# Performance work log

Hardware: AMD Instinct MI355X
Metric: run time of the kernel (lower is better)

The kernel has to match this reference:

```python
import jax, jax.numpy as jnp
import numpy as np

B, L, C = 256, 256, 128
HID, H = 128, 4
D = HID // H            # 32
NUM_LAYERS = 2
NEG_SLOPE = 0.2
LN_EPS = 1e-5


def setup_inputs() -> dict:
    key = jax.random.key(0)
    ks = jax.random.split(key, 16)
    E = 4096
    x = jax.random.normal(ks[0], (B, L, C), dtype=jnp.float32)
    edge_index = jax.random.randint(ks[1], (2, E), 0, C, dtype=jnp.int64)
    s_in = 1.0 / np.sqrt(L)
    s_h = 1.0 / np.sqrt(HID)
    return {
        "x": x,
        "edge_index": edge_index,
        "emb_W": jax.random.normal(ks[2], (L, HID), jnp.float32) * s_in,
        "emb_b": jnp.zeros((HID,), jnp.float32),
        "lin_l_W": jax.random.normal(ks[3], (NUM_LAYERS, HID, HID), jnp.float32) * s_h,
        "lin_l_b": jnp.zeros((NUM_LAYERS, HID), jnp.float32),
        "lin_r_W": jax.random.normal(ks[4], (NUM_LAYERS, HID, HID), jnp.float32) * s_h,
        "lin_r_b": jnp.zeros((NUM_LAYERS, HID), jnp.float32),
        "att": jax.random.normal(ks[5], (NUM_LAYERS, H, D), jnp.float32) * (1.0 / np.sqrt(D)),
        "gat_bias": jnp.zeros((NUM_LAYERS, HID), jnp.float32),
        "ln_gamma": jnp.ones((NUM_LAYERS, HID), jnp.float32),
        "ln_beta": jnp.zeros((NUM_LAYERS, HID), jnp.float32),
        "proj_W": jax.random.normal(ks[6], (HID, L), jnp.float32) * s_h,
        "proj_b": jnp.zeros((L,), jnp.float32),
    }


def _batch_edges(edge_index):
    # replicate single-graph edges per batch sample with node offsets, then add self loops
    E = edge_index.shape[1]
    off = jnp.repeat(jnp.arange(B, dtype=edge_index.dtype) * C, E)
    src = jnp.tile(edge_index[0], B) + off
    dst = jnp.tile(edge_index[1], B) + off
    loop = jnp.arange(B * C, dtype=edge_index.dtype)
    return jnp.concatenate([src, loop]), jnp.concatenate([dst, loop])


def _layer_norm(x, g, b):
    mu = jnp.mean(x, axis=-1, keepdims=True)
    var = jnp.mean(jnp.square(x - mu), axis=-1, keepdims=True)
    return (x - mu) * jax.lax.rsqrt(var + LN_EPS) * g + b


def _gatv2(x, src, dst, Wl, bl, Wr, br, a, bias):
    N = x.shape[0]
    xl = (x @ Wl + bl).reshape(N, H, D)   # source-side transform
    xr = (x @ Wr + br).reshape(N, H, D)   # target-side transform
    e = jax.nn.leaky_relu(xl[src] + xr[dst], NEG_SLOPE)   # (E', H, D)
    logits = jnp.einsum('ehd,hd->eh', e, a)               # (E', H)
    m = jax.ops.segment_max(logits, dst, num_segments=N)
    p = jnp.exp(logits - m[dst])
    s = jax.ops.segment_sum(p, dst, num_segments=N)
    alpha = p / (s[dst] + 1e-16)
    out = jax.ops.segment_sum(xl[src] * alpha[:, :, None], dst, num_segments=N)
    return out.reshape(N, HID) + bias, alpha


def reference(x, edge_index, emb_W, emb_b, lin_l_W, lin_l_b, lin_r_W, lin_r_b,
              att, gat_bias, ln_gamma, ln_beta, proj_W, proj_b):
    src, dst = _batch_edges(edge_index)
    # (B, L, C) -> nodes are channels: (B*C, L) -> embed to HID
    h = x.transpose(0, 2, 1).reshape(B * C, L) @ emb_W + emb_b
    alpha = None
    for i in range(NUM_LAYERS):
        new_h, alpha = _gatv2(h, src, dst, lin_l_W[i], lin_l_b[i],
                              lin_r_W[i], lin_r_b[i], att[i], gat_bias[i])
        new_h = jax.nn.elu(new_h)
        h = h + new_h
        h = _layer_norm(h, ln_gamma[i], ln_beta[i])
        # dropout: eval mode, identity
    # attention map (to_dense_adj semantics: adj[b, src%C, dst%C] = mean_h(alpha), then transpose)
    b_idx = src // C
    dense = jnp.zeros((B, C, C), x.dtype).at[b_idx, src % C, dst % C].add(alpha.mean(axis=-1))
    attn_map = dense.transpose(0, 2, 1)
    out = (h @ proj_W + proj_b).reshape(B, C, L).transpose(0, 2, 1)  # (B, L, C)
    return out, attn_map
```

## Files before the change

### kernel.cpp

```cpp
#include <hip/hip_runtime.h>
#include <hip/hip_fp16.h>
#include <math.h>

#define BB 256
#define LL 256
#define CC 128
#define HIDD 128
#define HH 4
#define DD 32
#define EE 4096
#define NN (BB*CC)
#define LN_EPS 1e-5f

typedef short bf16x8 __attribute__((ext_vector_type(8)));
typedef _Float16 f16x8 __attribute__((ext_vector_type(8)));
typedef float f32x4 __attribute__((ext_vector_type(4)));

__device__ __forceinline__ float red64(float p) {
    p += __shfl_xor(p, 32);
    p += __shfl_xor(p, 16);
    p += __shfl_xor(p, 8);
    p += __shfl_xor(p, 4);
    p += __shfl_xor(p, 2);
    p += __shfl_xor(p, 1);
    return p;
}
__device__ __forceinline__ unsigned bfr(float f) {
    unsigned x = __float_as_uint(f);
    return (x + 0x7FFFu + ((x >> 16) & 1u)) >> 16;
}
__device__ __forceinline__ unsigned pack2(float a, float b) { return bfr(a) | (bfr(b) << 16); }
__device__ __forceinline__ float b2f(unsigned u) { return __uint_as_float(u << 16); }

__device__ __forceinline__ void stage_bf16_rm(ushort* lds, const ushort* src, int ldm, int t) {
    #pragma unroll
    for (int i = 0; i < 8; ++i) {
        int flat = i*256 + t;
        int r = flat >> 4, c = flat & 15;
        uint4 pk = *(const uint4*)(src + (size_t)r*ldm + c*8);
        *(uint4*)&lds[((r*16) + (c ^ (r & 7)))*8] = pk;
    }
}
__device__ __forceinline__ void mfma_tile_128(const ushort* Als, const ushort* Bls,
                                              f32x4 acc[2][8], int w, int lane) {
    int mr = lane & 15, quad = lane >> 4;
    #pragma unroll
    for (int ks = 0; ks < 4; ++ks) {
        int ca = ks*4 + quad;
        bf16x8 a[2], b[8];
        #pragma unroll
        for (int mf = 0; mf < 2; ++mf) {
            int m = w*32 + mf*16 + mr;
            a[mf] = *(const bf16x8*)&Als[((m*16) + (ca ^ (m & 7)))*8];
        }
        #pragma unroll
        for (int nf = 0; nf < 8; ++nf) {
            int n = nf*16 + mr;
            b[nf] = *(const bf16x8*)&Bls[((n*16) + (ca ^ (n & 7)))*8];
        }
        #pragma unroll
        for (int mf = 0; mf < 2; ++mf)
            #pragma unroll
            for (int nf = 0; nf < 8; ++nf)
                acc[mf][nf] = __builtin_amdgcn_mfma_f32_16x16x32_bf16(a[mf], b[nf], acc[mf][nf], 0, 0, 0);
    }
}
#define ZERO_ACC(acc) { _Pragma("unroll") for (int i_=0;i_<2;++i_) { _Pragma("unroll") for (int j_=0;j_<8;++j_) acc[i_][j_] = (f32x4){0.f,0.f,0.f,0.f}; } }

__global__ __launch_bounds__(256) void prep_weights(const float* __restrict__ emb_W,
                                                    const float* __restrict__ lWl,
                                                    const float* __restrict__ lWr,
                                                    const float* __restrict__ pW,
                                                    const int* __restrict__ edge,
                                                    ushort* __restrict__ WembT,
                                                    ushort* __restrict__ WlrT,
                                                    ushort* __restrict__ WpT,
                                                    __half* __restrict__ mult_ds) {
    __shared__ int cnt[CC*CC];
    int t = threadIdx.x;
    if (blockIdx.x == 64) {
        for (int i = t; i < CC*CC; i += 256) cnt[i] = 0;
        __syncthreads();
        for (int j = t; j < EE; j += 256) {
            int s = edge[j], d = edge[EE + j];
            atomicAdd(&cnt[s*CC + d], 1);
        }
        __syncthreads();
        for (int o = t; o < CC*CC; o += 256) {
            int dstc = o >> 7, srcc = o & 127;
            int c = cnt[srcc*CC + dstc] + ((srcc == dstc) ? 1 : 0);
            mult_ds[o] = __float2half((float)c);
        }
        return;
    }
    int gid = blockIdx.x * 256 + t;
    float v[8];
    if (gid < 4096) {
        int f = gid >> 5, ch = gid & 31;
        #pragma unroll
        for (int j = 0; j < 8; ++j) v[j] = emb_W[(size_t)(ch*8 + j)*HIDD + f];
        uint4 pk; pk.x = pack2(v[0],v[1]); pk.y = pack2(v[2],v[3]);
        pk.z = pack2(v[4],v[5]); pk.w = pack2(v[6],v[7]);
        *(uint4*)&WembT[(size_t)f*LL + ch*8] = pk;
    } else if (gid < 12288) {
        int g = gid - 4096;
        int mat = g >> 11, f = (g >> 4) & 127, ch = g & 15;
        const float* src = ((mat & 1) ? lWr : lWl) + (size_t)(mat >> 1)*HIDD*HIDD;
        #pragma unroll
        for (int j = 0; j < 8; ++j) v[j] = src[(size_t)(ch*8 + j)*HIDD + f];
        uint4 pk; pk.x = pack2(v[0],v[1]); pk.y = pack2(v[2],v[3]);
        pk.z = pack2(v[4],v[5]); pk.w = pack2(v[6],v[7]);
        *(uint4*)&WlrT[(size_t)mat*HIDD*HIDD + (size_t)f*HIDD + ch*8] = pk;
    } else {
        int g = gid - 12288;
        int l = g >> 4, ch = g & 15;
        #pragma unroll
        for (int j = 0; j < 8; ++j) v[j] = pW[(size_t)(ch*8 + j)*LL + l];
        uint4 pk; pk.x = pack2(v[0],v[1]); pk.y = pack2(v[2],v[3]);
        pk.z = pack2(v[4],v[5]); pk.w = pack2(v[6],v[7]);
        *(uint4*)&WpT[(size_t)l*HIDD + ch*8] = pk;
    }
}

__global__ __launch_bounds__(256) void embed_mfma(const float* __restrict__ x,
                                                  const ushort* __restrict__ WembT,
                                                  const float* __restrict__ bias,
                                                  ushort* __restrict__ hout) {
    __shared__ __align__(16) ushort Als[128*16*8];
    __shared__ __align__(16) ushort Bls[128*16*8];
    int b = blockIdx.x;
    int t = threadIdx.x, lane = t & 63, w = t >> 6;
    f32x4 acc[2][8];
    ZERO_ACC(acc)
    #pragma unroll
    for (int kh = 0; kh < 2; ++kh) {
        if (kh) __syncthreads();
        const float4* x4 = (const float4*)(x + (size_t)b*LL*CC + (size_t)kh*128*CC);
        int rot = (t >> 3) & 3;
        #pragma unroll
        for (int i = 0; i < 8; ++i) {
            int flat = i*256 + t;
            int lp = flat >> 5, c4 = flat & 31;
            float4 v0 = x4[(size_t)(2*lp)*32 + c4];
            float4 v1 = x4[(size_t)(2*lp + 1)*32 + c4];
            int lc = lp >> 2, lh = lp & 3;
            #pragma unroll
            for (int j0 = 0; j0 < 4; ++j0) {
                int j = (j0 + rot) & 3;
                int c = c4*4 + j;
                unsigned pk = pack2(((const float*)&v0)[j], ((const float*)&v1)[j]);
                *(unsigned*)&Als[((c*16) + (lc ^ (c & 7)))*8 + lh*2] = pk;
            }
        }
        stage_bf16_rm(Bls, WembT + kh*128, LL, t);
        __syncthreads();
        mfma_tile_128(Als, Bls, acc, w, lane);
    }
    int mr = lane & 15, quad = lane >> 4;
    #pragma unroll
    for (int nf = 0; nf < 8; ++nf) {
        int f = nf*16 + mr;
        float bv = bias[f];
        #pragma unroll
        for (int mf = 0; mf < 2; ++mf)
            #pragma unroll
            for (int r = 0; r < 4; ++r) {
                int node = w*32 + mf*16 + quad*4 + r;
                hout[((size_t)b*CC + node)*HIDD + f] = (ushort)bfr(acc[mf][nf][r] + bv);
            }
    }
}

__global__ __launch_bounds__(256) void lin_mfma(const ushort* __restrict__ hmat,
                                                const ushort* __restrict__ WlT,
                                                const ushort* __restrict__ WrT,
                                                const float* __restrict__ bl,
                                                const float* __restrict__ br,
                                                __half* __restrict__ xlT,
                                                __half* __restrict__ xrT) {
    __shared__ __align__(16) ushort Als[128*16*8];
    __shared__ __align__(16) ushort Bls[128*16*8];
    int b = blockIdx.x;
    int t = threadIdx.x, lane = t & 63, w = t >> 6;
    int mr = lane & 15, quad = lane >> 4;
    stage_bf16_rm(Als, hmat + (size_t)b*CC*HIDD, HIDD, t);
    #pragma unroll
    for (int lr = 0; lr < 2; ++lr) {
        if (lr) __syncthreads();
        stage_bf16_rm(Bls, lr ? WrT : WlT, HIDD, t);
        __syncthreads();
        f32x4 acc[2][8];
        ZERO_ACC(acc)
        mfma_tile_128(Als, Bls, acc, w, lane);
        const float* bias = lr ? br : bl;
        __half* out = lr ? xrT : xlT;
        #pragma unroll
        for (int nf = 0; nf < 8; ++nf) {
            int f = nf*16 + mr;
            float bv = bias[f];
            int h = f >> 5, d = f & 31;
            #pragma unroll
            for (int mf = 0; mf < 2; ++mf)
                #pragma unroll
                for (int r = 0; r < 4; ++r) {
                    int node = w*32 + mf*16 + quad*4 + r;
                    out[(((size_t)b*HH + h)*CC + node)*DD + d] = __float2half(acc[mf][nf][r] + bv);
                }
        }
    }
}

#define SLOT(q, mr) ((mr)*4 + (((q) ^ (mr) ^ ((mr) >> 2)) & 3))

__global__ __launch_bounds__(256) __attribute__((amdgpu_waves_per_eu(4, 4)))
void gat_fused(const __half* __restrict__ xl_h,
               const __half* __restrict__ xr_h,
               const __half* __restrict__ mult_ds,
               const float* __restrict__ att,
               __half* __restrict__ xagg,
               __half* __restrict__ Pg) {
    __shared__ __align__(16) __half smemA[CC*CC];
    __shared__ __align__(16) __half xlT_swz[DD*16*8];
    __half* xl_lds = smemA;
    float*  Slq    = (float*)(smemA + CC*DD);
    float*  rp     = Slq + CC;
    float*  sp     = rp + 4*CC;
    __half* Pfrag  = smemA;

    int bh = blockIdx.x;
    int h = bh & 3, b = bh >> 2;
    int t = threadIdx.x;
    int sg = t >> 6, dl = t & 63;
    int dstA = dl, dstB = dl + 64;

    {
        const uint4* spg = (const uint4*)(xl_h + (size_t)bh * CC * DD);
        uint4* dp = (uint4*)xl_lds;
        dp[t] = spg[t];
        dp[t + 256] = spg[t + 256];
    }
    __half2 qa2[16];
    const float* ag = att + h*DD;
    #pragma unroll
    for (int c = 0; c < 8; ++c) {
        float4 av = *(const float4*)&ag[c*4];
        qa2[2*c+0] = __floats2half2_rn(0.4f*av.x, 0.4f*av.y);
        qa2[2*c+1] = __floats2half2_rn(0.4f*av.z, 0.4f*av.w);
    }
    __half2 xrA[16], xrB[16];
    float fSA, fSB;
    {
        uint4 XA[4], XB[4];
        const uint4* pa = (const uint4*)(xr_h + ((size_t)bh*CC + dstA)*DD);
        const uint4* pb = (const uint4*)(xr_h + ((size_t)bh*CC + dstB)*DD);
        #pragma unroll
        for (int c = 0; c < 4; ++c) { XA[c] = pa[c]; XB[c] = pb[c]; }
        const __half2* va = (const __half2*)XA;
        const __half2* vb = (const __half2*)XB;
        float sA = 0.f, sB = 0.f;
        #pragma unroll
        for (int i = 0; i < 16; ++i) {
            xrA[i] = va[i]; xrB[i] = vb[i];
            __half2 p = __hmul2(qa2[i], xrA[i]);
            sA += __low2float(p) + __high2float(p);
            __half2 q = __hmul2(qa2[i], xrB[i]);
            sB += __low2float(q) + __high2float(q);
        }
        fSA = 1.5f * sA; fSB = 1.5f * sB;
    }
    __syncthreads();

    if (t < CC) {
        uint4 R[4];
        const uint4* rpt = (const uint4*)&xl_lds[t*DD];
        #pragma unroll
        for (int c = 0; c < 4; ++c) R[c] = rpt[c];
        const __half2* rv = (const __half2*)R;
        __half2 s = __floats2half2_rn(0.f, 0.f);
        #pragma unroll
        for (int i = 0; i < 16; ++i) s = __hfma2(qa2[i], rv[i], s);
        Slq[t] = 1.5f * (__low2float(s) + __high2float(s));
    }
    for (int i = t; i < 512; i += 256) {
        int f = i & 31, c = i >> 5;
        __align__(16) __half v[8];
        #pragma unroll
        for (int e = 0; e < 8; ++e) v[e] = xl_lds[(c*8 + e)*DD + f];
        *(uint4*)&xlT_swz[((f*16) + (c ^ (f & 7)))*8] = *(uint4*)v;
    }
    __syncthreads();

    __half2 lvA[16], lvB[16];
    float pmA0 = -3.0e38f, pmA1 = pmA0, pmB0 = pmA0, pmB1 = pmA0;
    float lbufA = 0.f, lbufB = 0.f;
    #pragma unroll
    for (int j = 0; j < 32; ++j) {
        int src = sg*32 + j;
        uint4 R[4];
        const uint4* rpt = (const uint4*)&xl_lds[src*DD];
        R[0] = rpt[0]; R[1] = rpt[1]; R[2] = rpt[2]; R[3] = rpt[3];
        float sl = Slq[src];
        const __half2* xv = (const __half2*)R;
        __half2 a0 = __floats2half2_rn(0.f,0.f), a1 = a0, a2 = a0, a3 = a0;
        __half2 b0 = a0, b1 = a0, b2 = a0, b3 = a0;
        #pragma unroll
        for (int q = 0; q < 4; ++q) {
            a0 = __hfma2(qa2[4*q+0], __habs2(__hadd2(xv[4*q+0], xrA[4*q+0])), a0);
            a1 = __hfma2(qa2[4*q+1], __habs2(__hadd2(xv[4*q+1], xrA[4*q+1])), a1);
            a2 = __hfma2(qa2[4*q+2], __habs2(__hadd2(xv[4*q+2], xrA[4*q+2])), a2);
            a3 = __hfma2(qa2[4*q+3], __habs2(__hadd2(xv[4*q+3], xrA[4*q+3])), a3);
            b0 = __hfma2(qa2[4*q+0], __habs2(__hadd2(xv[4*q+0], xrB[4*q+0])), b0);
            b1 = __hfma2(qa2[4*q+1], __habs2(__hadd2(xv[4*q+1], xrB[4*q+1])), b1);
            b2 = __hfma2(qa2[4*q+2], __habs2(__hadd2(xv[4*q+2], xrB[4*q+2])), b2);
            b3 = __hfma2(qa2[4*q+3], __habs2(__hadd2(xv[4*q+3], xrB[4*q+3])), b3);
        }
        __half2 tsA = __hadd2(__hadd2(a0, a1), __hadd2(a2, a3));
        __half2 tsB = __hadd2(__hadd2(b0, b1), __hadd2(b2, b3));
        float lA = (fSA + sl) + (__low2float(tsA) + __high2float(tsA));
        float lB = (fSB + sl) + (__low2float(tsB) + __high2float(tsB));
        if (j & 1) {
            pmA1 = fmaxf(pmA1, lA); pmB1 = fmaxf(pmB1, lB);
            lvA[j >> 1] = __floats2half2_rn(lbufA, lA);
            lvB[j >> 1] = __floats2half2_rn(lbufB, lB);
        } else {
            pmA0 = fmaxf(pmA0, lA); pmB0 = fmaxf(pmB0, lB);
            lbufA = lA; lbufB = lB;
        }
    }
    rp[sg*CC + dstA] = fmaxf(pmA0, pmA1);
    rp[sg*CC + dstB] = fmaxf(pmB0, pmB1);
    __syncthreads();
    float mA = fmaxf(fmaxf(rp[0*CC + dstA], rp[1*CC + dstA]),
                     fmaxf(rp[2*CC + dstA], rp[3*CC + dstA]));
    float mB = fmaxf(fmaxf(rp[0*CC + dstB], rp[1*CC + dstB]),
                     fmaxf(rp[2*CC + dstB], rp[3*CC + dstB]));

    uint4 MAr[4], MBr[4];
    {
        const uint4* ma = (const uint4*)(mult_ds + (size_t)dstA*CC + sg*32);
        const uint4* mb = (const uint4*)(mult_ds + (size_t)dstB*CC + sg*32);
        #pragma unroll
        for (int c = 0; c < 4; ++c) { MAr[c] = ma[c]; MBr[c] = mb[c]; }
    }
    const __half* multA = (const __half*)MAr;
    const __half* multB = (const __half*)MBr;

    float sA0 = 0.f, sA1 = 0.f, sB0 = 0.f, sB1 = 0.f;
    #pragma unroll
    for (int i = 0; i < 16; ++i) {
        float eA0 = __expf(__low2float(lvA[i]) - mA) * __half2float(multA[2*i]);
        float eA1 = __expf(__high2float(lvA[i]) - mA) * __half2float(multA[2*i+1]);
        float eB0 = __expf(__low2float(lvB[i]) - mB) * __half2float(multB[2*i]);
        float eB1 = __expf(__high2float(lvB[i]) - mB) * __half2float(multB[2*i+1]);
        if (i & 1) { sA1 += eA0 + eA1; sB1 += eB0 + eB1; }
        else       { sA0 += eA0 + eA1; sB0 += eB0 + eB1; }
        lvA[i] = __floats2half2_rn(eA0, eA1);
        lvB[i] = __floats2half2_rn(eB0, eB1);
    }
    sp[sg*CC + dstA] = sA0 + sA1;
    sp[sg*CC + dstB] = sB0 + sB1;
    __syncthreads();
    float isA = 1.f / (((sp[0*CC + dstA] + sp[1*CC + dstA]) +
                        (sp[2*CC + dstA] + sp[3*CC + dstA])) + 1e-16f);
    float isB = 1.f / (((sp[0*CC + dstB] + sp[1*CC + dstB]) +
                        (sp[2*CC + dstB] + sp[3*CC + dstB])) + 1e-16f);
    __syncthreads();

    {
        int mr = dl & 15, dr0 = dl >> 4;
        __half* pfA = &Pfrag[(((dr0    )*4 + sg)*64)*8];
        __half* pfB = &Pfrag[(((dr0 + 4)*4 + sg)*64)*8];
        __half* pgA = Pg ? Pg + (size_t)bh*CC*CC + (size_t)dstA*CC + sg*32 : nullptr;
        __half* pgB = Pg ? Pg + (size_t)bh*CC*CC + (size_t)dstB*CC + sg*32 : nullptr;
        #pragma unroll
        for (int q = 0; q < 4; ++q) {
            __align__(16) __half ovA[8], ovB[8];
            #pragma unroll
            for (int i = 0; i < 4; ++i) {
                __half2 vA = lvA[q*4 + i], vB = lvB[q*4 + i];
                ovA[2*i+0] = __float2half(__low2float(vA) * isA);
                ovA[2*i+1] = __float2half(__high2float(vA) * isA);
                ovB[2*i+0] = __float2half(__low2float(vB) * isB);
                ovB[2*i+1] = __float2half(__high2float(vB) * isB);
            }
            *(uint4*)&pfA[SLOT(q, mr)*8] = *(uint4*)ovA;
            *(uint4*)&pfB[SLOT(q, mr)*8] = *(uint4*)ovB;
            if (pgA) {
                *(uint4*)&pgA[q*8] = *(uint4*)ovA;
                *(uint4*)&pgB[q*8] = *(uint4*)ovB;
            }
        }
    }
    __syncthreads();

    int quad = dl >> 4, mr = dl & 15;
    f16x8 afr[2][4];
    #pragma unroll
    for (int mf = 0; mf < 2; ++mf) {
        int dr0 = sg*2 + mf;
        #pragma unroll
        for (int ks = 0; ks < 4; ++ks)
            afr[mf][ks] = *(const f16x8*)&Pfrag[((dr0*4 + ks)*64 + SLOT(quad, mr))*8];
    }
    f32x4 acc[2][2];
    #pragma unroll
    for (int i = 0; i < 2; ++i)
        #pragma unroll
        for (int j = 0; j < 2; ++j) acc[i][j] = (f32x4){0.f,0.f,0.f,0.f};
    #pragma unroll
    for (int ks = 0; ks < 4; ++ks) {
        int ca = ks*4 + quad;
        f16x8 bfr2[2];
        #pragma unroll
        for (int nf = 0; nf < 2; ++nf) {
            int n = nf*16 + mr;
            bfr2[nf] = *(const f16x8*)&xlT_swz[((n*16) + (ca ^ (n & 7)))*8];
        }
        #pragma unroll
        for (int mf = 0; mf < 2; ++mf)
            #pragma unroll
            for (int nf = 0; nf < 2; ++nf)
                acc[mf][nf] = __builtin_amdgcn_mfma_f32_16x16x32_f16(afr[mf][ks], bfr2[nf], acc[mf][nf], 0, 0, 0);
    }
    #pragma unroll
    for (int mf = 0; mf < 2; ++mf)
        #pragma unroll
        for (int nf = 0; nf < 2; ++nf) {
            int f = nf*16 + mr;
            #pragma unroll
            for (int r = 0; r < 4; ++r) {
                int node = sg*32 + mf*16 + quad*4 + r;
                xagg[(((size_t)b*CC + node)*HH + h)*DD + f] = __float2half(acc[mf][nf][r]);
            }
        }
}

__global__ __launch_bounds__(256) void gat_epilogue(const __half* __restrict__ xagg,
                                                    const float* __restrict__ gbias,
                                                    const float* __restrict__ ln_g,
                                                    const float* __restrict__ ln_b,
                                                    const __half* __restrict__ Pws,
                                                    ushort* __restrict__ hmat,
                                                    float* __restrict__ attn_out) {
    int t = threadIdx.x;
    int w = t >> 6, lane = t & 63;
    int node = blockIdx.x*4 + w;
    int b = node >> 7, dstc = node & 127;
    int f0 = lane*2;

    __half2 xa = *(const __half2*)&xagg[(size_t)node*HIDD + f0];
    unsigned hp = *(const unsigned*)&hmat[(size_t)node*HIDD + f0];
    float2 gb = *(const float2*)&gbias[f0];
    float o0 = __low2float(xa) + gb.x;
    float o1 = __high2float(xa) + gb.y;
    o0 = o0 > 0.f ? o0 : (__expf(o0) - 1.f);
    o1 = o1 > 0.f ? o1 : (__expf(o1) - 1.f);
    float hv0 = b2f(hp & 0xFFFFu) + o0;
    float hv1 = b2f(hp >> 16) + o1;

    float mean = red64(hv0 + hv1) * 0.0078125f;
    float d0 = hv0 - mean, d1 = hv1 - mean;
    float var = red64(d0*d0 + d1*d1) * 0.0078125f;
    float rs = rsqrtf(var + LN_EPS);
    float2 g2 = *(const float2*)&ln_g[f0];
    float2 be = *(const float2*)&ln_b[f0];
    *(unsigned*)&hmat[(size_t)node*HIDD + f0] =
        pack2(d0*rs*g2.x + be.x, d1*rs*g2.y + be.y);

    if (attn_out) {
        float a0 = 0.f, a1 = 0.f;
        #pragma unroll
        for (int hh = 0; hh < HH; ++hh) {
            __half2 v = *(const __half2*)&Pws[((size_t)(b*HH + hh)*CC + dstc)*CC + f0];
            a0 += __low2float(v);
            a1 += __high2float(v);
        }
        float2 o; o.x = 0.25f*a0; o.y = 0.25f*a1;
        *(float2*)&attn_out[(size_t)node*CC + f0] = o;
    }
}

__global__ __launch_bounds__(256) void proj_mfma(const ushort* __restrict__ hmat,
                                                 const ushort* __restrict__ WpT,
                                                 const float* __restrict__ bias,
                                                 float* __restrict__ out) {
    __shared__ __align__(16) ushort Als[128*16*8];
    __shared__ __align__(16) ushort Bls[128*16*8];
    int l0 = blockIdx.x * 128;
    int b  = blockIdx.y;
    int t = threadIdx.x, lane = t & 63, w = t >> 6;
    f32x4 acc[2][8];
    ZERO_ACC(acc)
    stage_bf16_rm(Als, WpT + (size_t)l0*HIDD, HIDD, t);
    stage_bf16_rm(Bls, hmat + (size_t)b*CC*HIDD, HIDD, t);
    __syncthreads();
    mfma_tile_128(Als, Bls, acc, w, lane);
    int mr = lane & 15, quad = lane >> 4;
    #pragma unroll
    for (int nf = 0; nf < 8; ++nf) {
        int c = nf*16 + mr;
        #pragma unroll
        for (int mf = 0; mf < 2; ++mf)
            #pragma unroll
            for (int r = 0; r < 4; ++r) {
                int l = l0 + w*32 + mf*16 + quad*4 + r;
                out[((size_t)b*LL + l)*CC + c] = acc[mf][nf][r] + bias[l];
            }
    }
}

extern "C" void kernel_launch(void* const* d_in, const int* in_sizes, int n_in,
                              void* d_out, int out_size, void* d_ws, size_t ws_size,
                              hipStream_t stream) {
    const float* x        = (const float*)d_in[0];
    const int*   edge     = (const int*)d_in[1];
    const float* emb_W    = (const float*)d_in[2];
    const float* emb_b    = (const float*)d_in[3];
    const float* lin_l_W  = (const float*)d_in[4];
    const float* lin_l_b  = (const float*)d_in[5];
    const float* lin_r_W  = (const float*)d_in[6];
    const float* lin_r_b  = (const float*)d_in[7];
    const float* att      = (const float*)d_in[8];
    const float* gat_bias = (const float*)d_in[9];
    const float* ln_g     = (const float*)d_in[10];
    const float* ln_b     = (const float*)d_in[11];
    const float* proj_W   = (const float*)d_in[12];
    const float* proj_b   = (const float*)d_in[13];

    ushort* h     = (ushort*)d_ws;
    __half* xl_h  = (__half*)(h + (size_t)NN * HIDD);
    __half* xr_h  = xl_h + (size_t)NN * HIDD;
    __half* xagg  = xr_h + (size_t)NN * HIDD;
    __half* Pg    = xagg + (size_t)NN * HIDD;
    __half* mult_ds = Pg + (size_t)BB * HH * CC * CC;
    ushort* WembT = (ushort*)(mult_ds + (size_t)CC * CC);
    ushort* WlrT  = WembT + (size_t)CC*LL;
    ushort* WpT   = WlrT + (size_t)4*HIDD*HIDD;

    float* out0 = (float*)d_out;
    float* attn = out0 + (size_t)BB * LL * CC;

    prep_weights<<<65, 256, 0, stream>>>(emb_W, lin_l_W, lin_r_W, proj_W, edge,
                                         WembT, WlrT, WpT, mult_ds);
    embed_mfma<<<BB, 256, 0, stream>>>(x, WembT, emb_b, h);
    for (int layer = 0; layer < 2; ++layer) {
        lin_mfma<<<BB, 256, 0, stream>>>(h,
            WlrT + (size_t)(layer*2 + 0)*HIDD*HIDD,
            WlrT + (size_t)(layer*2 + 1)*HIDD*HIDD,
            lin_l_b + layer*HIDD, lin_r_b + layer*HIDD,
            xl_h, xr_h);
        gat_fused<<<BB*HH, 256, 0, stream>>>(xl_h, xr_h, mult_ds,
            att + layer*HIDD, xagg, (layer == 1) ? Pg : nullptr);
        gat_epilogue<<<NN/4, 256, 0, stream>>>(xagg,
            gat_bias + layer*HIDD, ln_g + layer*HIDD, ln_b + layer*HIDD,
            (layer == 1) ? Pg : nullptr, h, (layer == 1) ? attn : nullptr);
    }
    proj_mfma<<<dim3(2, BB), 256, 0, stream>>>(h, WpT, proj_b, out0);
}
```

Measured before the change: 288.3 us.

## Fuse GAT epilogue LayerNorm into following linear and projection kernels

Result: slower. 401.5 us (+39.3%).

```diff
diff --git a/kernel.cpp b/kernel.cpp
--- a/kernel.cpp
+++ b/kernel.cpp
@@ -16,15 +16,6 @@
 typedef _Float16 f16x8 __attribute__((ext_vector_type(8)));
 typedef float f32x4 __attribute__((ext_vector_type(4)));
 
-__device__ __forceinline__ float red64(float p) {
-    p += __shfl_xor(p, 32);
-    p += __shfl_xor(p, 16);
-    p += __shfl_xor(p, 8);
-    p += __shfl_xor(p, 4);
-    p += __shfl_xor(p, 2);
-    p += __shfl_xor(p, 1);
-    return p;
-}
 __device__ __forceinline__ unsigned bfr(float f) {
     unsigned x = __float_as_uint(f);
     return (x + 0x7FFFu + ((x >> 16) & 1u)) >> 16;
@@ -66,6 +57,75 @@
     }
 }
 #define ZERO_ACC(acc) { _Pragma("unroll") for (int i_=0;i_<2;++i_) { _Pragma("unroll") for (int j_=0;j_<8;++j_) acc[i_][j_] = (f32x4){0.f,0.f,0.f,0.f}; } }
+
+__device__ __forceinline__ void epilogue_to_tile(const __half* __restrict__ xagg,
+                                                 const float* __restrict__ gbias,
+                                                 const float* __restrict__ ln_g,
+                                                 const float* __restrict__ ln_b,
+                                                 ushort* __restrict__ hmat,
+                                                 ushort* __restrict__ tile,
+                                                 int b, int t, bool write_h) {
+    int nl = t >> 1, fh = t & 1;
+    int node = b*CC + nl;
+    const __half* xa = xagg + (size_t)node*HIDD + fh*64;
+    ushort* hp = hmat + (size_t)node*HIDD + fh*64;
+    const float* gb = gbias + fh*64;
+
+    __half2 hv[32];
+    float sum = 0.f;
+    #pragma unroll
+    for (int c = 0; c < 8; ++c) {
+        uint4 xu = *(const uint4*)&xa[c*8];
+        uint4 hu = *(const uint4*)&hp[c*8];
+        const __half2* xp2 = (const __half2*)&xu;
+        const ushort* hs = (const ushort*)&hu;
+        float gv[8];
+        *(float4*)&gv[0] = *(const float4*)&gb[c*8];
+        *(float4*)&gv[4] = *(const float4*)&gb[c*8 + 4];
+        #pragma unroll
+        for (int i = 0; i < 4; ++i) {
+            float o0 = __low2float(xp2[i]) + gv[2*i];
+            float o1 = __high2float(xp2[i]) + gv[2*i+1];
+            o0 = o0 > 0.f ? o0 : (__expf(o0) - 1.f);
+            o1 = o1 > 0.f ? o1 : (__expf(o1) - 1.f);
+            float v0 = b2f((unsigned)hs[2*i]) + o0;
+            float v1 = b2f((unsigned)hs[2*i+1]) + o1;
+            sum += v0 + v1;
+            hv[c*4 + i] = __floats2half2_rn(v0, v1);
+        }
+    }
+    float mean = (sum + __shfl_xor(sum, 1)) * 0.0078125f;
+    float q = 0.f;
+    #pragma unroll
+    for (int i = 0; i < 32; ++i) {
+        float d0 = __low2float(hv[i]) - mean;
+        float d1 = __high2float(hv[i]) - mean;
+        q += d0*d0 + d1*d1;
+    }
+    float var = (q + __shfl_xor(q, 1)) * 0.0078125f;
+    float rs = rsqrtf(var + LN_EPS);
+    const float* lg = ln_g + fh*64;
+    const float* lb = ln_b + fh*64;
+    #pragma unroll
+    for (int c = 0; c < 8; ++c) {
+        float gv[8], bv[8];
+        *(float4*)&gv[0] = *(const float4*)&lg[c*8];
+        *(float4*)&gv[4] = *(const float4*)&lg[c*8 + 4];
+        *(float4*)&bv[0] = *(const float4*)&lb[c*8];
+        *(float4*)&bv[4] = *(const float4*)&lb[c*8 + 4];
+        __align__(16) ushort ov[8];
+        #pragma unroll
+        for (int i = 0; i < 4; ++i) {
+            float d0 = __low2float(hv[c*4 + i]) - mean;
+            float d1 = __high2float(hv[c*4 + i]) - mean;
+            ov[2*i]   = (ushort)bfr(d0*rs*gv[2*i]   + bv[2*i]);
+            ov[2*i+1] = (ushort)bfr(d1*rs*gv[2*i+1] + bv[2*i+1]);
+        }
+        int cg = fh*8 + c;
+        *(uint4*)&tile[((nl*16) + (cg ^ (nl & 7)))*8] = *(uint4*)ov;
+        if (write_h) *(uint4*)&hp[c*8] = *(uint4*)ov;
+    }
+}
 
 __global__ __launch_bounds__(256) void prep_weights(const float* __restrict__ emb_W,
                                                     const float* __restrict__ lWl,
@@ -171,6 +231,38 @@
     }
 }
 
+__device__ __forceinline__ void lin_body(ushort* Als, ushort* Bls,
+                                         const ushort* WlT, const ushort* WrT,
+                                         const float* bl, const float* br,
+                                         __half* xlT, __half* xrT, int b, int t) {
+    int lane = t & 63, w = t >> 6;
+    int mr = lane & 15, quad = lane >> 4;
+    #pragma unroll
+    for (int lr = 0; lr < 2; ++lr) {
+        if (lr) __syncthreads();
+        stage_bf16_rm(Bls, lr ? WrT : WlT, HIDD, t);
+        __syncthreads();
+        f32x4 acc[2][8];
+        ZERO_ACC(acc)
+        mfma_tile_128(Als, Bls, acc, w, lane);
+        const float* bias = lr ? br : bl;
+        __half* out = lr ? xrT : xlT;
+        #pragma unroll
+        for (int nf = 0; nf < 8; ++nf) {
+            int f = nf*16 + mr;
+            float bv = bias[f];
+            int h = f >> 5, d = f & 31;
+            #pragma unroll
+            for (int mf = 0; mf < 2; ++mf)
+                #pragma unroll
+                for (int r = 0; r < 4; ++r) {
+                    int node = w*32 + mf*16 + quad*4 + r;
+                    out[(((size_t)b*HH + h)*CC + node)*DD + d] = __float2half(acc[mf][nf][r] + bv);
+                }
+        }
+    }
+}
+
 __global__ __launch_bounds__(256) void lin_mfma(const ushort* __restrict__ hmat,
                                                 const ushort* __restrict__ WlT,
                                                 const ushort* __restrict__ WrT,
@@ -180,39 +272,32 @@
                                                 __half* __restrict__ xrT) {
     __shared__ __align__(16) ushort Als[128*16*8];
     __shared__ __align__(16) ushort Bls[128*16*8];
-    int b = blockIdx.x;
-    int t = threadIdx.x, lane = t & 63, w = t >> 6;
-    int mr = lane & 15, quad = lane >> 4;
+    int b = blockIdx.x, t = threadIdx.x;
     stage_bf16_rm(Als, hmat + (size_t)b*CC*HIDD, HIDD, t);
-    #pragma unroll
-    for (int lr = 0; lr < 2; ++lr) {
-        if (lr) __syncthreads();
-        stage_bf16_rm(Bls, lr ? WrT : WlT, HIDD, t);
-        __syncthreads();
-        f32x4 acc[2][8];
-        ZERO_ACC(acc)
-        mfma_tile_128(Als, Bls, acc, w, lane);
-        const float* bias = lr ? br : bl;
-        __half* out = lr ? xrT : xlT;
-        #pragma unroll
-        for (int nf = 0; nf < 8; ++nf) {
-            int f = nf*16 + mr;
-            float bv = bias[f];
-            int h = f >> 5, d = f & 31;
-            #pragma unroll
-            for (int mf = 0; mf < 2; ++mf)
-                #pragma unroll
-                for (int r = 0; r < 4; ++r) {
-                    int node = w*32 + mf*16 + quad*4 + r;
-                    out[(((size_t)b*HH + h)*CC + node)*DD + d] = __float2half(acc[mf][nf][r] + bv);
-                }
-        }
-    }
+    lin_body(Als, Bls, WlT, WrT, bl, br, xlT, xrT, b, t);
+}
+
+__global__ __launch_bounds__(256) void epi_lin(const __half* __restrict__ xagg,
+                                               const float* __restrict__ gbias,
+                                               const float* __restrict__ ln_g,
+                                               const float* __restrict__ ln_b,
+                                               const ushort* __restrict__ WlT,
+                                               const ushort* __restrict__ WrT,
+                                               const float* __restrict__ bl,
+                                               const float* __restrict__ br,
+                                               ushort* __restrict__ hmat,
+                                               __half* __restrict__ xlT,
+                                               __half* __restrict__ xrT) {
+    __shared__ __align__(16) ushort Als[128*16*8];
+    __shared__ __align__(16) ushort Bls[128*16*8];
+    int b = blockIdx.x, t = threadIdx.x;
+    epilogue_to_tile(xagg, gbias, ln_g, ln_b, hmat, Als, b, t, true);
+    lin_body(Als, Bls, WlT, WrT, bl, br, xlT, xrT, b, t);
 }
 
 #define SLOT(q, mr) ((mr)*4 + (((q) ^ (mr) ^ ((mr) >> 2)) & 3))
 
-__global__ __launch_bounds__(256) __attribute__((amdgpu_waves_per_eu(4, 4)))
+__global__ __launch_bounds__(256) __attribute__((amdgpu_num_vgpr(128)))
 void gat_fused(const __half* __restrict__ xl_h,
                const __half* __restrict__ xr_h,
                const __half* __restrict__ mult_ds,
@@ -435,77 +520,66 @@
         }
 }
 
-__global__ __launch_bounds__(256) void gat_epilogue(const __half* __restrict__ xagg,
-                                                    const float* __restrict__ gbias,
-                                                    const float* __restrict__ ln_g,
-                                                    const float* __restrict__ ln_b,
-                                                    const __half* __restrict__ Pws,
-                                                    ushort* __restrict__ hmat,
-                                                    float* __restrict__ attn_out) {
-    int t = threadIdx.x;
-    int w = t >> 6, lane = t & 63;
-    int node = blockIdx.x*4 + w;
-    int b = node >> 7, dstc = node & 127;
-    int f0 = lane*2;
-
-    __half2 xa = *(const __half2*)&xagg[(size_t)node*HIDD + f0];
-    unsigned hp = *(const unsigned*)&hmat[(size_t)node*HIDD + f0];
-    float2 gb = *(const float2*)&gbias[f0];
-    float o0 = __low2float(xa) + gb.x;
-    float o1 = __high2float(xa) + gb.y;
-    o0 = o0 > 0.f ? o0 : (__expf(o0) - 1.f);
-    o1 = o1 > 0.f ? o1 : (__expf(o1) - 1.f);
-    float hv0 = b2f(hp & 0xFFFFu) + o0;
-    float hv1 = b2f(hp >> 16) + o1;
-
-    float mean = red64(hv0 + hv1) * 0.0078125f;
-    float d0 = hv0 - mean, d1 = hv1 - mean;
-    float var = red64(d0*d0 + d1*d1) * 0.0078125f;
-    float rs = rsqrtf(var + LN_EPS);
-    float2 g2 = *(const float2*)&ln_g[f0];
-    float2 be = *(const float2*)&ln_b[f0];
-    *(unsigned*)&hmat[(size_t)node*HIDD + f0] =
-        pack2(d0*rs*g2.x + be.x, d1*rs*g2.y + be.y);
-
-    if (attn_out) {
-        float a0 = 0.f, a1 = 0.f;
-        #pragma unroll
-        for (int hh = 0; hh < HH; ++hh) {
-            __half2 v = *(const __half2*)&Pws[((size_t)(b*HH + hh)*CC + dstc)*CC + f0];
-            a0 += __low2float(v);
-            a1 += __high2float(v);
-        }
-        float2 o; o.x = 0.25f*a0; o.y = 0.25f*a1;
-        *(float2*)&attn_out[(size_t)node*CC + f0] = o;
-    }
-}
-
-__global__ __launch_bounds__(256) void proj_mfma(const ushort* __restrict__ hmat,
-                                                 const ushort* __restrict__ WpT,
-                                                 const float* __restrict__ bias,
-                                                 float* __restrict__ out) {
+__global__ __launch_bounds__(256) void epi_proj(const __half* __restrict__ xagg,
+                                                const float* __restrict__ gbias,
+                                                const float* __restrict__ ln_g,
+                                                const float* __restrict__ ln_b,
+                                                const __half* __restrict__ Pg,
+                                                const ushort* __restrict__ WpT,
+                                                const float* __restrict__ pbias,
+                                                ushort* __restrict__ hmat,
+                                                float* __restrict__ out,
+                                                float* __restrict__ attn_out) {
     __shared__ __align__(16) ushort Als[128*16*8];
     __shared__ __align__(16) ushort Bls[128*16*8];
-    int l0 = blockIdx.x * 128;
-    int b  = blockIdx.y;
-    int t = threadIdx.x, lane = t & 63, w = t >> 6;
-    f32x4 acc[2][8];
-    ZERO_ACC(acc)
-    stage_bf16_rm(Als, WpT + (size_t)l0*HIDD, HIDD, t);
-    stage_bf16_rm(Bls, hmat + (size_t)b*CC*HIDD, HIDD, t);
-    __syncthreads();
-    mfma_tile_128(Als, Bls, acc, w, lane);
+    int b = blockIdx.x, t = threadIdx.x;
+    epilogue_to_tile(xagg, gbias, ln_g, ln_b, hmat, Bls, b, t, false);
+
+    {
+        int nl = t >> 1, fh = t & 1;
+        int node = b*CC + nl;
+        #pragma unroll
+        for (int c = 0; c < 8; ++c) {
+            float a[8] = {0.f,0.f,0.f,0.f,0.f,0.f,0.f,0.f};
+            #pragma unroll
+            for (int hh = 0; hh < HH; ++hh) {
+                uint4 pu = *(const uint4*)&Pg[((size_t)(b*HH + hh)*CC + nl)*CC + fh*64 + c*8];
+                const __half2* pv = (const __half2*)&pu;
+                #pragma unroll
+                for (int i = 0; i < 4; ++i) {
+                    a[2*i]   += __low2float(pv[i]);
+                    a[2*i+1] += __high2float(pv[i]);
+                }
+            }
+            float4 o0, o1;
+            o0.x = 0.25f*a[0]; o0.y = 0.25f*a[1]; o0.z = 0.25f*a[2]; o0.w = 0.25f*a[3];
+            o1.x = 0.25f*a[4]; o1.y = 0.25f*a[5]; o1.z = 0.25f*a[6]; o1.w = 0.25f*a[7];
+            *(float4*)&attn_out[(size_t)node*CC + fh*64 + c*8]     = o0;
+            *(float4*)&attn_out[(size_t)node*CC + fh*64 + c*8 + 4] = o1;
+        }
+    }
+
+    int lane = t & 63, w = t >> 6;
     int mr = lane & 15, quad = lane >> 4;
     #pragma unroll
-    for (int nf = 0; nf < 8; ++nf) {
-        int c = nf*16 + mr;
-        #pragma unroll
-        for (int mf = 0; mf < 2; ++mf)
-            #pragma unroll
-            for (int r = 0; r < 4; ++r) {
-                int l = l0 + w*32 + mf*16 + quad*4 + r;
-                out[((size_t)b*LL + l)*CC + c] = acc[mf][nf][r] + bias[l];
-            }
+    for (int half = 0; half < 2; ++half) {
+        __syncthreads();
+        stage_bf16_rm(Als, WpT + (size_t)half*128*HIDD, HIDD, t);
+        __syncthreads();
+        f32x4 acc[2][8];
+        ZERO_ACC(acc)
+        mfma_tile_128(Als, Bls, acc, w, lane);
+        #pragma unroll
+        for (int nf = 0; nf < 8; ++nf) {
+            int c = nf*16 + mr;
+            #pragma unroll
+            for (int mf = 0; mf < 2; ++mf)
+                #pragma unroll
+                for (int r = 0; r < 4; ++r) {
+                    int l = half*128 + w*32 + mf*16 + quad*4 + r;
+                    out[((size_t)b*LL + l)*CC + c] = acc[mf][nf][r] + pbias[l];
+                }
+        }
     }
 }
 
@@ -543,17 +617,15 @@
     prep_weights<<<65, 256, 0, stream>>>(emb_W, lin_l_W, lin_r_W, proj_W, edge,
                                          WembT, WlrT, WpT, mult_ds);
     embed_mfma<<<BB, 256, 0, stream>>>(x, WembT, emb_b, h);
-    for (int layer = 0; layer < 2; ++layer) {
-        lin_mfma<<<BB, 256, 0, stream>>>(h,
-            WlrT + (size_t)(layer*2 + 0)*HIDD*HIDD,
-            WlrT + (size_t)(layer*2 + 1)*HIDD*HIDD,
-            lin_l_b + layer*HIDD, lin_r_b + layer*HIDD,
-            xl_h, xr_h);
-        gat_fused<<<BB*HH, 256, 0, stream>>>(xl_h, xr_h, mult_ds,
-            att + layer*HIDD, xagg, (layer == 1) ? Pg : nullptr);
-        gat_epilogue<<<NN/4, 256, 0, stream>>>(xagg,
-            gat_bias + layer*HIDD, ln_g + layer*HIDD, ln_b + layer*HIDD,
-            (layer == 1) ? Pg : nullptr, h, (layer == 1) ? attn : nullptr);
-    }
-    proj_mfma<<<dim3(2, BB), 256, 0, stream>>>(h, WpT, proj_b, out0);
-}
+    lin_mfma<<<BB, 256, 0, stream>>>(h, WlrT, WlrT + (size_t)HIDD*HIDD,
+                                     lin_l_b, lin_r_b, xl_h, xr_h);
+    gat_fused<<<BB*HH, 256, 0, stream>>>(xl_h, xr_h, mult_ds, att, xagg, nullptr);
+    epi_lin<<<BB, 256, 0, stream>>>(xagg, gat_bias, ln_g, ln_b,
+                                    WlrT + (size_t)2*HIDD*HIDD,
+                                    WlrT + (size_t)3*HIDD*HIDD,
+                                    lin_l_b + HIDD, lin_r_b + HIDD,
+                                    h, xl_h, xr_h);
+    gat_fused<<<BB*HH, 256, 0, stream>>>(xl_h, xr_h, mult_ds, att + HIDD, xagg, Pg);
+    epi_proj<<<BB, 256, 0, stream>>>(xagg, gat_bias + HIDD, ln_g + HIDD, ln_b + HIDD,
+                                     Pg, WpT, proj_b, h, out0, attn);
+}
```
